# Performance work log

Measured on AMD Instinct MI355X. Metric: run time of the kernel, lower is better.

Reference implementation:

```python
import jax, jax.numpy as jnp
import numpy as np


def setup_inputs() -> dict:
    key = jax.random.key(0)
    k1, k2, k3 = jax.random.split(key, 3)
    B, C, H, W = 8, 256, 64, 64
    K = jax.random.normal(k1, (B, C, H, W), dtype=jnp.float32)
    Q = jax.random.normal(k2, (B, C, H, W), dtype=jnp.float32)
    V = jax.random.normal(k3, (B, C, H, W), dtype=jnp.float32)
    return {"K": K, "Q": Q, "V": V}


def reference(K, Q, V):
    # K, Q: [b, dim, h, w]; V: [b, v_dim, h, w]
    b, dim, h, w = K.shape
    v_dim = V.shape[1]
    hw = h * w
    Qf = jnp.transpose(K.reshape(b, dim, hw), (0, 2, 1)) * 0  # placeholder removed below
    Qf = jnp.transpose(Q.reshape(b, dim, hw), (0, 2, 1))  # [b, hw, dim]
    Kf = K.reshape(b, dim, hw)                              # [b, dim, hw]
    Vf = jnp.transpose(V.reshape(b, v_dim, hw), (0, 2, 1))  # [b, hw, v_dim]
    scores = jnp.einsum('bqd,bdk->bqk', Qf, Kf)             # [b, hw_q, hw_k]
    # NOTE: softmax over the QUERY axis (dim=1), matching the torch code
    att = jax.nn.softmax(scores, axis=1)
    out = jnp.einsum('bqk,bkv->bqv', att, Vf)               # [b, hw, v_dim]
    out = out.reshape(b, h, w, v_dim)
    return jnp.transpose(out, (0, 3, 1, 2))                 # [b, v_dim, h, w]
```

## Files before the change

kernel.cpp:

```cpp
#include <hip/hip_runtime.h>

#define HW   4096
#define DIM  256
#define NB   8

typedef short bf16x8 __attribute__((ext_vector_type(8)));
typedef short s16x4  __attribute__((ext_vector_type(4)));
typedef float f32x4  __attribute__((ext_vector_type(4)));
typedef float f32x16 __attribute__((ext_vector_type(16)));
typedef unsigned int u32;
typedef unsigned int u32_g __attribute__((address_space(1)));
typedef unsigned int u32_l __attribute__((address_space(3)));

__device__ __forceinline__ void split_bf16(float x, short& hi, short& lo) {
    unsigned u  = __builtin_bit_cast(unsigned, x);
    unsigned rh = (u + 0x7FFFu + ((u >> 16) & 1u)) >> 16;
    hi = (short)rh;
    float hf  = __builtin_bit_cast(float, rh << 16);
    float rem = x - hf;
    unsigned u2 = __builtin_bit_cast(unsigned, rem);
    unsigned rl = (u2 + 0x7FFFu + ((u2 >> 16) & 1u)) >> 16;
    lo = (short)rl;
}

__device__ __forceinline__ f32x4 mfma16(bf16x8 a, bf16x8 b, f32x4 c) {
    return __builtin_amdgcn_mfma_f32_16x16x32_bf16(a, b, c, 0, 0, 0);
}
__device__ __forceinline__ f32x16 mfma32(bf16x8 a, bf16x8 b, f32x16 c) {
    return __builtin_amdgcn_mfma_f32_32x32x16_bf16(a, b, c, 0, 0, 0);
}

__device__ __forceinline__ void gload16(const void* g, void* l) {
    __builtin_amdgcn_global_load_lds((const u32_g*)g, (u32_l*)l, 16, 0, 0);
}

extern "C" __global__ void __launch_bounds__(256)
pass0_T(const float* __restrict__ src, short* __restrict__ dsth,
        short* __restrict__ dstl)
{
    __shared__ __attribute__((aligned(16))) short TH[16][264];
    __shared__ __attribute__((aligned(16))) short TL[16][264];
    const int b   = blockIdx.y;
    const int hw0 = blockIdx.x * 16;
    const int t   = threadIdx.x;
    const float* sb = src + (size_t)b * DIM * HW;

    {
        const int rl = t & 15;
        const int dl = t >> 4;
        #pragma unroll
        for (int dp = 0; dp < 16; ++dp) {
            int d = dl + dp * 16;
            float x = sb[(size_t)d * HW + hw0 + rl];
            short h, l; split_bf16(x, h, l);
            TH[rl][d] = h; TL[rl][d] = l;
        }
    }
    __syncthreads();

    const int r   = t >> 4;
    const int c0  = (t & 15) * 2;
    const int swz = (r & 7) << 4;
    size_t rowbyte = ((size_t)b * HW + hw0 + r) * (size_t)(DIM * 2);
    char* dh = (char*)dsth + rowbyte;
    char* dl = (char*)dstl + rowbyte;
    #pragma unroll
    for (int j = 0; j < 2; ++j) {
        int cb  = (c0 + j) * 16;
        int cbs = cb ^ swz;
        *(f32x4*)(dh + cbs) = *(const f32x4*)((const char*)&TH[r][0] + cb);
        *(f32x4*)(dl + cbs) = *(const f32x4*)((const char*)&TL[r][0] + cb);
    }
}

extern "C" __global__ void __launch_bounds__(256)
pass0_V(const float* __restrict__ V, short* __restrict__ v2)
{
    const int b = blockIdx.y, v = blockIdx.x, t = threadIdx.x;
    const float* sv = V + ((size_t)b * DIM + v) * HW + t * 16;
    #pragma unroll
    for (int s = 0; s < 2; ++s) {
        f32x4 x0 = *(const f32x4*)(sv + s * 8);
        f32x4 x1 = *(const f32x4*)(sv + s * 8 + 4);
        s16x4 h0, l0, h1, l1;
        #pragma unroll
        for (int j = 0; j < 4; ++j) {
            short h, l;
            split_bf16(x0[j], h, l); h0[j] = h; l0[j] = l;
            split_bf16(x1[j], h, l); h1[j] = h; l1[j] = l;
        }
        short* dp = v2 + (((size_t)b * 512 + (size_t)(t * 2 + s)) * DIM + v) * 16;
        *(s16x4*)(dp + 0)  = h0;
        *(s16x4*)(dp + 4)  = h1;
        *(s16x4*)(dp + 8)  = l0;
        *(s16x4*)(dp + 12) = l1;
    }
}

extern "C" __global__ void __launch_bounds__(512, 2)
k3_stats(const short* __restrict__ KTh, const short* __restrict__ KTl,
         const short* __restrict__ QTh, const short* __restrict__ QTl,
         float* __restrict__ m_out, float* __restrict__ il_out)
{
    __shared__ __attribute__((aligned(16))) short QH[2][64][256];
    __shared__ __attribute__((aligned(16))) short QL[2][64][256];

    const int id   = blockIdx.x;
    const int b    = id & 7;
    const int k0b  = (id >> 3) * 128;
    const int t    = threadIdx.x;
    const int lane = t & 63;
    const int w    = t >> 6;
    const int g    = lane >> 4;
    const int lq   = lane & 15;

    bf16x8 kh[8], kl[8];
    {
        const int krow = k0b + w * 16 + lq;
        const char* rh = (const char*)KTh + ((size_t)b * HW + krow) * 512;
        const char* rl = (const char*)KTl + ((size_t)b * HW + krow) * 512;
        const int swz = (lq & 7) << 4;
        #pragma unroll
        for (int ds = 0; ds < 8; ++ds) {
            int cb = (64 * ds + 16 * g) ^ swz;
            kh[ds] = *(const bf16x8*)(rh + cb);
            kl[ds] = *(const bf16x8*)(rl + cb);
        }
    }

    const char* qhbase = (const char*)QTh + (size_t)b * HW * 512;
    const char* qlbase = (const char*)QTl + (size_t)b * HW * 512;
    auto stage = [&](int bi, int q0) {
        #pragma unroll
        for (int j = 0; j < 4; ++j) {
            int c = (j << 3) + w;
            int o = c * 1024;
            gload16(qhbase + (size_t)q0 * 512 + o + lane * 16,
                    (char*)&QH[bi][0][0] + o);
            gload16(qlbase + (size_t)q0 * 512 + o + lane * 16,
                    (char*)&QL[bi][0][0] + o);
        }
    };

    float mr[4], lr[4];
    #pragma unroll
    for (int r = 0; r < 4; ++r) { mr[r] = -3.0e38f; lr[r] = 0.0f; }

    stage(0, 0);
    __syncthreads();

    for (int it = 0; it < 64; ++it) {
        const int cur = it & 1;
        if (it + 1 < 64) stage(cur ^ 1, (it + 1) * 64);

        #pragma unroll
        for (int qt = 0; qt < 4; ++qt) {
            const int qr = qt * 16 + lq;
            const char* bhr = (const char*)&QH[cur][qr][0];
            const char* blr = (const char*)&QL[cur][qr][0];
            const int swzq = (qr & 7) << 4;
            f32x4 acc = {0.f, 0.f, 0.f, 0.f};
            __builtin_amdgcn_s_setprio(1);
            #pragma unroll
            for (int ds = 0; ds < 8; ++ds) {
                int cb = (64 * ds + 16 * g) ^ swzq;
                bf16x8 bh = *(const bf16x8*)(bhr + cb);
                bf16x8 bl = *(const bf16x8*)(blr + cb);
                acc = mfma16(kh[ds], bh, acc);
                acc = mfma16(kh[ds], bl, acc);
                acc = mfma16(kl[ds], bh, acc);
            }
            __builtin_amdgcn_s_setprio(0);
            #pragma unroll
            for (int r = 0; r < 4; ++r) {
                float s = acc[r];
                if (s > mr[r]) {
                    lr[r] = lr[r] * __expf(mr[r] - s) + 1.0f;
                    mr[r] = s;
                } else {
                    lr[r] += __expf(s - mr[r]);
                }
            }
        }
        __syncthreads();
    }

    #pragma unroll
    for (int r = 0; r < 4; ++r) {
        float m = mr[r], l = lr[r];
        #pragma unroll
        for (int off = 1; off < 16; off <<= 1) {
            float m2 = __shfl_xor(m, off);
            float l2 = __shfl_xor(l, off);
            float mn = fmaxf(m, m2);
            l = l * __expf(m - mn) + l2 * __expf(m2 - mn);
            m = mn;
        }
        if (lq == 0) {
            int kg = k0b + w * 16 + g * 4 + r;
            m_out[b * HW + kg]  = m;
            il_out[b * HW + kg] = 1.0f / l;
        }
    }
}

extern "C" __global__ void __launch_bounds__(512, 2)
k3_out(const short* __restrict__ KTh, const short* __restrict__ KTl,
       const short* __restrict__ QTh, const short* __restrict__ QTl,
       const short* __restrict__ V2,
       const float* __restrict__ m_in, const float* __restrict__ il_in,
       float* __restrict__ out)
{
    __shared__ __attribute__((aligned(16))) short KH[2][32][256];
    __shared__ __attribute__((aligned(16))) short KL[2][32][256];
    __shared__ __attribute__((aligned(16))) short PH[2][128][36];
    __shared__ __attribute__((aligned(16))) short PL[2][128][36];

    const int id   = blockIdx.x;
    const int b    = id & 7;
    const int q0   = (id >> 3) * 128;
    const int t    = threadIdx.x;
    const int lane = t & 63;
    const int w    = t >> 6;
    const int g    = lane >> 4;
    const int lq   = lane & 15;
    const int g2   = lane >> 5;
    const int l32  = lane & 31;
    const int wv   = w >> 1;
    const int wq2  = w & 1;

    bf16x8 qh[8], ql[8];
    {
        const int qrow = q0 + w * 16 + lq;
        const char* rh = (const char*)QTh + ((size_t)b * HW + qrow) * 512;
        const char* rl = (const char*)QTl + ((size_t)b * HW + qrow) * 512;
        const int swz = (lq & 7) << 4;
        #pragma unroll
        for (int ds = 0; ds < 8; ++ds) {
            int cb = (64 * ds + 16 * g) ^ swz;
            qh[ds] = *(const bf16x8*)(rh + cb);
            ql[ds] = *(const bf16x8*)(rl + cb);
        }
    }

    const char* khbase = (const char*)KTh + (size_t)b * HW * 512;
    const char* klbase = (const char*)KTl + (size_t)b * HW * 512;
    auto stage = [&](int bi, int k0a) {
        #pragma unroll
        for (int j = 0; j < 2; ++j) {
            int c = (j << 3) + w;
            int o = c * 1024;
            gload16(khbase + (size_t)k0a * 512 + o + lane * 16,
                    (char*)&KH[bi][0][0] + o);
            gload16(klbase + (size_t)k0a * 512 + o + lane * 16,
                    (char*)&KL[bi][0][0] + o);
        }
    };

    f32x16 acc[2][2];
    #pragma unroll
    for (int i = 0; i < 2; ++i)
        #pragma unroll
        for (int j = 0; j < 2; ++j)
            #pragma unroll
            for (int e = 0; e < 16; ++e) acc[i][j][e] = 0.0f;

    const float* mB  = m_in  + b * HW;
    const float* ilB = il_in + b * HW;

    stage(0, 0);
    __syncthreads();

    for (int it = 0; it < 128; ++it) {
        const int cur = it & 1;
        const int k0  = it * 32;

        if (it + 1 < 128) stage(cur ^ 1, k0 + 32);

        f32x4 mv[2], iv[2];
        #pragma unroll
        for (int kt = 0; kt < 2; ++kt) {
            mv[kt] = *(const f32x4*)&mB[k0 + kt * 16 + g * 4];
            iv[kt] = *(const f32x4*)&ilB[k0 + kt * 16 + g * 4];
        }

        bf16x8 vfh[2][2], vfl[2][2];
        #pragma unroll
        for (int kc = 0; kc < 2; ++kc) {
            const int seg = (k0 >> 3) + kc * 2 + g2;
            #pragma unroll
            for (int mt = 0; mt < 2; ++mt) {
                const int v = wv * 64 + mt * 32 + l32;
                const short* vp = V2 + (((size_t)b * 512 + seg) * DIM + v) * 16;
                vfh[kc][mt] = *(const bf16x8*)(vp);
                vfl[kc][mt] = *(const bf16x8*)(vp + 8);
            }
        }

        f32x4 sacc[2];
        #pragma unroll
        for (int kt = 0; kt < 2; ++kt) { f32x4 z = {0.f,0.f,0.f,0.f}; sacc[kt] = z; }
        const int swzk = (lq & 7) << 4;
        const char* ahr0 = (const char*)&KH[cur][lq][0];
        const char* ahr1 = (const char*)&KH[cur][16 + lq][0];
        const char* alr0 = (const char*)&KL[cur][lq][0];
        const char* alr1 = (const char*)&KL[cur][16 + lq][0];
        __builtin_amdgcn_s_setprio(1);
        #pragma unroll
        for (int ds = 0; ds < 8; ++ds) {
            int cb = (64 * ds + 16 * g) ^ swzk;
            {
                bf16x8 ah = *(const bf16x8*)(ahr0 + cb);
                bf16x8 al = *(const bf16x8*)(alr0 + cb);
                sacc[0] = mfma16(ah, qh[ds], sacc[0]);
                sacc[0] = mfma16(ah, ql[ds], sacc[0]);
                sacc[0] = mfma16(al, qh[ds], sacc[0]);
            }
            {
                bf16x8 ah = *(const bf16x8*)(ahr1 + cb);
                bf16x8 al = *(const bf16x8*)(alr1 + cb);
                sacc[1] = mfma16(ah, qh[ds], sacc[1]);
                sacc[1] = mfma16(ah, ql[ds], sacc[1]);
                sacc[1] = mfma16(al, qh[ds], sacc[1]);
            }
        }
        __builtin_amdgcn_s_setprio(0);

        {
            const int qc = w * 16 + lq;
            #pragma unroll
            for (int kt = 0; kt < 2; ++kt) {
                s16x4 ph, pl;
                #pragma unroll
                for (int r = 0; r < 4; ++r) {
                    float p = __expf(sacc[kt][r] - mv[kt][r]) * iv[kt][r];
                    short h, l; split_bf16(p, h, l);
                    ph[r] = h; pl[r] = l;
                }
                *(s16x4*)&PH[cur][qc][kt * 16 + g * 4] = ph;
                *(s16x4*)&PL[cur][qc][kt * 16 + g * 4] = pl;
            }
        }

        __syncthreads();

        __builtin_amdgcn_s_setprio(1);
        #pragma unroll
        for (int kc = 0; kc < 2; ++kc) {
            bf16x8 pbh[2], pbl[2];
            #pragma unroll
            for (int qt = 0; qt < 2; ++qt) {
                const int prow = wq2 * 64 + qt * 32 + l32;
                const short* p0 = &PH[cur][prow][kc * 16 + g2 * 8];
                const short* p1 = &PL[cur][prow][kc * 16 + g2 * 8];
                s16x4 a0 = *(const s16x4*)(p0);
                s16x4 a1 = *(const s16x4*)(p0 + 4);
                s16x4 b0 = *(const s16x4*)(p1);
                s16x4 b1 = *(const s16x4*)(p1 + 4);
                bf16x8 rh, rl;
                #pragma unroll
                for (int e = 0; e < 4; ++e) {
                    rh[e] = a0[e]; rh[4 + e] = a1[e];
                    rl[e] = b0[e]; rl[4 + e] = b1[e];
                }
                pbh[qt] = rh; pbl[qt] = rl;
            }
            #pragma unroll
            for (int mt = 0; mt < 2; ++mt) {
                #pragma unroll
                for (int qt = 0; qt < 2; ++qt) {
                    acc[mt][qt] = mfma32(vfh[kc][mt], pbh[qt], acc[mt][qt]);
                    acc[mt][qt] = mfma32(vfh[kc][mt], pbl[qt], acc[mt][qt]);
                    acc[mt][qt] = mfma32(vfl[kc][mt], pbh[qt], acc[mt][qt]);
                }
            }
        }
        __builtin_amdgcn_s_setprio(0);
    }

    float* __restrict__ ob = out + (size_t)b * DIM * HW;
    #pragma unroll
    for (int mt = 0; mt < 2; ++mt)
        #pragma unroll
        for (int qt = 0; qt < 2; ++qt)
            #pragma unroll
            for (int r = 0; r < 16; ++r) {
                int v = wv * 64 + mt * 32 + (r & 3) + 8 * (r >> 2) + 4 * g2;
                int q = q0 + wq2 * 64 + qt * 32 + l32;
                ob[(size_t)v * HW + q] = acc[mt][qt][r];
            }
}

extern "C" __global__ void __launch_bounds__(256, 1)
k_stats(const float* __restrict__ K, const float* __restrict__ Q,
        float* __restrict__ m_out, float* __restrict__ il_out)
{
    __shared__ __attribute__((aligned(16))) short KtH[64][264];
    __shared__ __attribute__((aligned(16))) short KtL[64][264];
    __shared__ __attribute__((aligned(16))) short QtH[32][264];
    __shared__ __attribute__((aligned(16))) short QtL[32][264];

    const int b = blockIdx.y, k0 = blockIdx.x * 64, t = threadIdx.x;
    const int lane = t & 63, w = t >> 6, g = lane >> 4, lq = lane & 15;
    const float* Kb = K + (size_t)b * DIM * HW;
    const float* Qb = Q + (size_t)b * DIM * HW;

    {
        const int kk = t & 63, d0 = t >> 6;
        #pragma unroll 4
        for (int pass = 0; pass < 64; ++pass) {
            int d = d0 + pass * 4;
            float x = Kb[(size_t)d * HW + k0 + kk];
            short h, l; split_bf16(x, h, l);
            KtH[kk][d] = h; KtL[kk][d] = l;
        }
    }
    float mr[4], lr[4];
    #pragma unroll
    for (int r = 0; r < 4; ++r) { mr[r] = -3.0e38f; lr[r] = 0.0f; }

    for (int q0 = 0; q0 < HW; q0 += 32) {
        __syncthreads();
        {
            const int qq = t & 31, d0 = t >> 5;
            #pragma unroll 4
            for (int pass = 0; pass < 32; ++pass) {
                int d = d0 + pass * 8;
                float x = Qb[(size_t)d * HW + q0 + qq];
                short h, l; split_bf16(x, h, l);
                QtH[qq][d] = h; QtL[qq][d] = l;
            }
        }
        __syncthreads();
        #pragma unroll
        for (int qt = 0; qt < 2; ++qt) {
            f32x4 acc = {0.f, 0.f, 0.f, 0.f};
            #pragma unroll
            for (int ds = 0; ds < 8; ++ds) {
                const int dof = ds * 32 + g * 8;
                bf16x8 ah = *(const bf16x8*)&KtH[w * 16 + lq][dof];
                bf16x8 al = *(const bf16x8*)&KtL[w * 16 + lq][dof];
                bf16x8 bh = *(const bf16x8*)&QtH[qt * 16 + lq][dof];
                bf16x8 bl = *(const bf16x8*)&QtL[qt * 16 + lq][dof];
                acc = mfma16(ah, bh, acc);
                acc = mfma16(ah, bl, acc);
                acc = mfma16(al, bh, acc);
            }
            #pragma unroll
            for (int r = 0; r < 4; ++r) {
                float s = acc[r];
                if (s > mr[r]) { lr[r] = lr[r] * __expf(mr[r] - s) + 1.0f; mr[r] = s; }
                else lr[r] += __expf(s - mr[r]);
            }
        }
    }
    #pragma unroll
    for (int r = 0; r < 4; ++r) {
        float m = mr[r], l = lr[r];
        #pragma unroll
        for (int off = 1; off < 16; off <<= 1) {
            float m2 = __shfl_xor(m, off), l2 = __shfl_xor(l, off);
            float mn = fmaxf(m, m2);
            l = l * __expf(m - mn) + l2 * __expf(m2 - mn);
            m = mn;
        }
        if (lq == 0) {
            int kg = k0 + w * 16 + g * 4 + r;
            m_out[b * HW + kg] = m;
            il_out[b * HW + kg] = 1.0f / l;
        }
    }
}

extern "C" __global__ void __launch_bounds__(256, 1)
k_attn_out(const float* __restrict__ K, const float* __restrict__ Q,
           const float* __restrict__ V,
           const float* __restrict__ m_in, const float* __restrict__ il_in,
           float* __restrict__ out)
{
    __shared__ __attribute__((aligned(16))) short QtH[64][264];
    __shared__ __attribute__((aligned(16))) short QtL[64][264];
    __shared__ __attribute__((aligned(16))) short KtH[32][264];
    __shared__ __attribute__((aligned(16))) short KtL[32][264];
    __shared__ __attribute__((aligned(16))) short PtH[64][40];
    __shared__ __attribute__((aligned(16))) short PtL[64][40];

    const int b = blockIdx.y, q0 = blockIdx.x * 64, t = threadIdx.x;
    const int lane = t & 63, w = t >> 6, g = lane >> 4, lq = lane & 15;
    const int g2 = lane >> 5, l32 = lane & 31;
    const float* Kb = K + (size_t)b * DIM * HW;
    const float* Qb = Q + (size_t)b * DIM * HW;
    const float* Vb = V + (size_t)b * DIM * HW;
    const float* mB = m_in + b * HW;
    const float* ilB = il_in + b * HW;

    {
        const int qq = t & 63, d0 = t >> 6;
        #pragma unroll 4
        for (int pass = 0; pass < 64; ++pass) {
            int d = d0 + pass * 4;
            float x = Qb[(size_t)d * HW + q0 + qq];
            short h, l; split_bf16(x, h, l);
            QtH[qq][d] = h; QtL[qq][d] = l;
        }
    }
    f32x16 acc[2][2];
    #pragma unroll
    for (int i = 0; i < 2; ++i)
        #pragma unroll
        for (int j = 0; j < 2; ++j)
            #pragma unroll
            for (int e = 0; e < 16; ++e) acc[i][j][e] = 0.0f;

    for (int k0 = 0; k0 < HW; k0 += 32) {
        __syncthreads();
        {
            const int kk = t & 31, d0 = t >> 5;
            #pragma unroll 4
            for (int pass = 0; pass < 32; ++pass) {
                int d = d0 + pass * 8;
                float x = Kb[(size_t)d * HW + k0 + kk];
                short h, l; split_bf16(x, h, l);
                KtH[kk][d] = h; KtL[kk][d] = l;
            }
        }
        __syncthreads();
        f32x4 sacc[2];
        #pragma unroll
        for (int kt = 0; kt < 2; ++kt) { f32x4 z = {0.f,0.f,0.f,0.f}; sacc[kt] = z; }
        #pragma unroll
        for (int ds = 0; ds < 8; ++ds) {
            const int dof = ds * 32 + g * 8;
            bf16x8 bh = *(const bf16x8*)&QtH[w * 16 + lq][dof];
            bf16x8 bl = *(const bf16x8*)&QtL[w * 16 + lq][dof];
            #pragma unroll
            for (int kt = 0; kt < 2; ++kt) {
                bf16x8 ah = *(const bf16x8*)&KtH[kt * 16 + lq][dof];
                bf16x8 al = *(const bf16x8*)&KtL[kt * 16 + lq][dof];
                sacc[kt] = mfma16(ah, bh, sacc[kt]);
                sacc[kt] = mfma16(ah, bl, sacc[kt]);
                sacc[kt] = mfma16(al, bh, sacc[kt]);
            }
        }
        {
            const int qc = w * 16 + lq;
            #pragma unroll
            for (int kt = 0; kt < 2; ++kt) {
                s16x4 ph, pl;
                #pragma unroll
                for (int r = 0; r < 4; ++r) {
                    int kg = k0 + kt * 16 + g * 4 + r;
                    float p = __expf(sacc[kt][r] - mB[kg]) * ilB[kg];
                    short h, l; split_bf16(p, h, l);
                    ph[r] = h; pl[r] = l;
                }
                *(s16x4*)&PtH[qc][kt * 16 + g * 4] = ph;
                *(s16x4*)&PtL[qc][kt * 16 + g * 4] = pl;
            }
        }
        __syncthreads();
        #pragma unroll
        for (int kc = 0; kc < 2; ++kc) {
            bf16x8 pbh[2], pbl[2];
            #pragma unroll
            for (int qt = 0; qt < 2; ++qt) {
                pbh[qt] = *(const bf16x8*)&PtH[qt * 32 + l32][kc * 16 + g2 * 8];
                pbl[qt] = *(const bf16x8*)&PtL[qt * 32 + l32][kc * 16 + g2 * 8];
            }
            #pragma unroll
            for (int mt = 0; mt < 2; ++mt) {
                const int v = w * 64 + mt * 32 + l32;
                const float* vp = Vb + (size_t)v * HW + k0 + kc * 16 + g2 * 8;
                f32x4 x0 = *(const f32x4*)vp;
                f32x4 x1 = *(const f32x4*)(vp + 4);
                bf16x8 ah, al;
                #pragma unroll
                for (int j = 0; j < 4; ++j) {
                    short h, l;
                    split_bf16(x0[j], h, l); ah[j] = h;     al[j] = l;
                    split_bf16(x1[j], h, l); ah[4 + j] = h; al[4 + j] = l;
                }
                #pragma unroll
                for (int qt = 0; qt < 2; ++qt) {
                    acc[mt][qt] = mfma32(ah, pbh[qt], acc[mt][qt]);
                    acc[mt][qt] = mfma32(ah, pbl[qt], acc[mt][qt]);
                    acc[mt][qt] = mfma32(al, pbh[qt], acc[mt][qt]);
                }
            }
        }
    }
    float* ob = out + (size_t)b * DIM * HW;
    #pragma unroll
    for (int mt = 0; mt < 2; ++mt)
        #pragma unroll
        for (int qt = 0; qt < 2; ++qt)
            #pragma unroll
            for (int r = 0; r < 16; ++r) {
                int v = w * 64 + mt * 32 + (r & 3) + 8 * (r >> 2) + 4 * g2;
                int q = q0 + qt * 32 + l32;
                ob[(size_t)v * HW + q] = acc[mt][qt][r];
            }
}

extern "C" void kernel_launch(void* const* d_in, const int* in_sizes, int n_in,
                              void* d_out, int out_size, void* d_ws, size_t ws_size,
                              hipStream_t stream)
{
    (void)in_sizes; (void)n_in; (void)out_size;
    const float* K = (const float*)d_in[0];
    const float* Q = (const float*)d_in[1];
    const float* V = (const float*)d_in[2];

    char* wsb = (char*)d_ws;
    float* m_ws  = (float*)wsb;
    float* il_ws = m_ws + (size_t)NB * HW;

    const size_t planeElems = (size_t)NB * HW * DIM;
    const size_t statsBytes = 262144;
    const size_t need = statsBytes + planeElems * 2 * 4
                                   + planeElems * 2 * 2 ;

    dim3 blk(256);
    if (ws_size >= need) {
        short* KTh = (short*)(wsb + statsBytes);
        short* KTl = KTh + planeElems;
        short* QTh = KTl + planeElems;
        short* QTl = QTh + planeElems;
        short* V2  = QTl + planeElems;

        dim3 gT(HW / 16, NB);
        pass0_T<<<gT, blk, 0, stream>>>(K, KTh, KTl);
        pass0_T<<<gT, blk, 0, stream>>>(Q, QTh, QTl);
        dim3 gV(DIM, NB);
        pass0_V<<<gV, blk, 0, stream>>>(V, V2);

        dim3 blk5(512);
        k3_stats<<<dim3(256), blk5, 0, stream>>>(KTh, KTl, QTh, QTl, m_ws, il_ws);
        k3_out<<<dim3(256), blk5, 0, stream>>>(KTh, KTl, QTh, QTl, V2,
                                               m_ws, il_ws, (float*)d_out);
    } else {
        dim3 gM(64, NB);
        k_stats<<<gM, blk, 0, stream>>>(K, Q, m_ws, il_ws);
        k_attn_out<<<gM, blk, 0, stream>>>(K, Q, V, m_ws, il_ws, (float*)d_out);
    }
}
```

Measured before the change: 638.3 us.

## Switch attention stats and output kernels to 32x32 MFMA tiles with larger K chunks

Both the stats and output kernels move their score GEMM from 16x16x32 to 32x32x16 MFMA tiles. Each wave now covers 32 keys by 32 queries and holds 16 register fragments per operand. The stats kernel adds an LDS merge of partial max/sum across two query-half waves. The output kernel processes 64 keys per iteration with a single-buffered K tile, loads m/il through async LDS loads, and reads P fragments with wider vector loads. The aim is fewer loop iterations, fewer LDS fragment reads per MFMA and better MFMA efficiency. The cost is higher register pressure and an extra barrier per iteration, since the K loads now follow the score compute instead of being double-buffered.

```diff
diff --git a/kernel.cpp b/kernel.cpp
--- a/kernel.cpp
+++ b/kernel.cpp
@@ -8,7 +8,6 @@
 typedef short s16x4  __attribute__((ext_vector_type(4)));
 typedef float f32x4  __attribute__((ext_vector_type(4)));
 typedef float f32x16 __attribute__((ext_vector_type(16)));
-typedef unsigned int u32;
 typedef unsigned int u32_g __attribute__((address_space(1)));
 typedef unsigned int u32_l __attribute__((address_space(3)));
 
@@ -32,6 +31,9 @@
 
 __device__ __forceinline__ void gload16(const void* g, void* l) {
     __builtin_amdgcn_global_load_lds((const u32_g*)g, (u32_l*)l, 16, 0, 0);
+}
+__device__ __forceinline__ void gload4(const void* g, void* l) {
+    __builtin_amdgcn_global_load_lds((const u32_g*)g, (u32_l*)l, 4, 0, 0);
 }
 
 extern "C" __global__ void __launch_bounds__(256)
@@ -98,12 +100,13 @@
 }
 
 extern "C" __global__ void __launch_bounds__(512, 2)
-k3_stats(const short* __restrict__ KTh, const short* __restrict__ KTl,
+k4_stats(const short* __restrict__ KTh, const short* __restrict__ KTl,
          const short* __restrict__ QTh, const short* __restrict__ QTl,
          float* __restrict__ m_out, float* __restrict__ il_out)
 {
     __shared__ __attribute__((aligned(16))) short QH[2][64][256];
     __shared__ __attribute__((aligned(16))) short QL[2][64][256];
+    __shared__ __attribute__((aligned(16))) float MRG[2][128][2];
 
     const int id   = blockIdx.x;
     const int b    = id & 7;
@@ -111,20 +114,22 @@
     const int t    = threadIdx.x;
     const int lane = t & 63;
     const int w    = t >> 6;
-    const int g    = lane >> 4;
-    const int lq   = lane & 15;
-
-    bf16x8 kh[8], kl[8];
+    const int l32  = lane & 31;
+    const int g2   = lane >> 5;
+    const int wk   = w >> 1;
+    const int wq   = w & 1;
+
+    bf16x8 kh[16], kl[16];
     {
-        const int krow = k0b + w * 16 + lq;
+        const int krow = k0b + wk * 32 + l32;
         const char* rh = (const char*)KTh + ((size_t)b * HW + krow) * 512;
         const char* rl = (const char*)KTl + ((size_t)b * HW + krow) * 512;
-        const int swz = (lq & 7) << 4;
-        #pragma unroll
-        for (int ds = 0; ds < 8; ++ds) {
-            int cb = (64 * ds + 16 * g) ^ swz;
-            kh[ds] = *(const bf16x8*)(rh + cb);
-            kl[ds] = *(const bf16x8*)(rl + cb);
+        const int swz = (l32 & 7) << 4;
+        #pragma unroll
+        for (int s = 0; s < 16; ++s) {
+            int cb = (s * 32 + g2 * 16) ^ swz;
+            kh[s] = *(const bf16x8*)(rh + cb);
+            kl[s] = *(const bf16x8*)(rl + cb);
         }
     }
 
@@ -133,8 +138,8 @@
     auto stage = [&](int bi, int q0) {
         #pragma unroll
         for (int j = 0; j < 4; ++j) {
-            int c = (j << 3) + w;
-            int o = c * 1024;
+            int cc = (j << 3) + w;
+            int o  = cc * 1024;
             gload16(qhbase + (size_t)q0 * 512 + o + lane * 16,
                     (char*)&QH[bi][0][0] + o);
             gload16(qlbase + (size_t)q0 * 512 + o + lane * 16,
@@ -142,79 +147,92 @@
         }
     };
 
-    float mr[4], lr[4];
-    #pragma unroll
-    for (int r = 0; r < 4; ++r) { mr[r] = -3.0e38f; lr[r] = 0.0f; }
+    float mr[16], lr[16];
+    #pragma unroll
+    for (int r = 0; r < 16; ++r) { mr[r] = -3.0e38f; lr[r] = 0.0f; }
 
     stage(0, 0);
     __syncthreads();
+
+    const int qrow = wq * 32 + l32;
+    const int qswz = (qrow & 7) << 4;
 
     for (int it = 0; it < 64; ++it) {
         const int cur = it & 1;
         if (it + 1 < 64) stage(cur ^ 1, (it + 1) * 64);
 
-        #pragma unroll
-        for (int qt = 0; qt < 4; ++qt) {
-            const int qr = qt * 16 + lq;
-            const char* bhr = (const char*)&QH[cur][qr][0];
-            const char* blr = (const char*)&QL[cur][qr][0];
-            const int swzq = (qr & 7) << 4;
-            f32x4 acc = {0.f, 0.f, 0.f, 0.f};
-            __builtin_amdgcn_s_setprio(1);
-            #pragma unroll
-            for (int ds = 0; ds < 8; ++ds) {
-                int cb = (64 * ds + 16 * g) ^ swzq;
-                bf16x8 bh = *(const bf16x8*)(bhr + cb);
-                bf16x8 bl = *(const bf16x8*)(blr + cb);
-                acc = mfma16(kh[ds], bh, acc);
-                acc = mfma16(kh[ds], bl, acc);
-                acc = mfma16(kl[ds], bh, acc);
-            }
-            __builtin_amdgcn_s_setprio(0);
-            #pragma unroll
-            for (int r = 0; r < 4; ++r) {
-                float s = acc[r];
-                if (s > mr[r]) {
-                    lr[r] = lr[r] * __expf(mr[r] - s) + 1.0f;
-                    mr[r] = s;
-                } else {
-                    lr[r] += __expf(s - mr[r]);
-                }
-            }
-        }
-        __syncthreads();
-    }
-
-    #pragma unroll
-    for (int r = 0; r < 4; ++r) {
+        const char* bhr = (const char*)&QH[cur][qrow][0];
+        const char* blr = (const char*)&QL[cur][qrow][0];
+        f32x16 c1, c2;
+        #pragma unroll
+        for (int e = 0; e < 16; ++e) { c1[e] = 0.0f; c2[e] = 0.0f; }
+
+        __builtin_amdgcn_s_setprio(1);
+        #pragma unroll
+        for (int s = 0; s < 16; ++s) {
+            int cb = (s * 32 + g2 * 16) ^ qswz;
+            bf16x8 bh = *(const bf16x8*)(bhr + cb);
+            bf16x8 bl = *(const bf16x8*)(blr + cb);
+            c1 = mfma32(kh[s], bh, c1);
+            c1 = mfma32(kh[s], bl, c1);
+            c2 = mfma32(kl[s], bh, c2);
+        }
+        __builtin_amdgcn_s_setprio(0);
+
+        #pragma unroll
+        for (int r = 0; r < 16; ++r) {
+            float sv = c1[r] + c2[r];
+            float nm = fmaxf(mr[r], sv);
+            lr[r] = lr[r] * __expf(mr[r] - nm) + __expf(sv - nm);
+            mr[r] = nm;
+        }
+        __syncthreads();
+    }
+
+    #pragma unroll
+    for (int r = 0; r < 16; ++r) {
         float m = mr[r], l = lr[r];
         #pragma unroll
-        for (int off = 1; off < 16; off <<= 1) {
+        for (int off = 1; off < 32; off <<= 1) {
             float m2 = __shfl_xor(m, off);
             float l2 = __shfl_xor(l, off);
-            float mn = fmaxf(m, m2);
-            l = l * __expf(m - mn) + l2 * __expf(m2 - mn);
-            m = mn;
-        }
-        if (lq == 0) {
-            int kg = k0b + w * 16 + g * 4 + r;
-            m_out[b * HW + kg]  = m;
-            il_out[b * HW + kg] = 1.0f / l;
-        }
+            float nm = fmaxf(m, m2);
+            l = l * __expf(m - nm) + l2 * __expf(m2 - nm);
+            m = nm;
+        }
+        mr[r] = m; lr[r] = l;
+    }
+    if (l32 == 0) {
+        #pragma unroll
+        for (int r = 0; r < 16; ++r) {
+            int klo = wk * 32 + 4 * g2 + (r & 3) + 8 * (r >> 2);
+            MRG[wq][klo][0] = mr[r];
+            MRG[wq][klo][1] = lr[r];
+        }
+    }
+    __syncthreads();
+    if (t < 128) {
+        float m0 = MRG[0][t][0], l0 = MRG[0][t][1];
+        float m1 = MRG[1][t][0], l1 = MRG[1][t][1];
+        float nm = fmaxf(m0, m1);
+        float l  = l0 * __expf(m0 - nm) + l1 * __expf(m1 - nm);
+        m_out[b * HW + k0b + t]  = nm;
+        il_out[b * HW + k0b + t] = 1.0f / l;
     }
 }
 
 extern "C" __global__ void __launch_bounds__(512, 2)
-k3_out(const short* __restrict__ KTh, const short* __restrict__ KTl,
+k4_out(const short* __restrict__ KTh, const short* __restrict__ KTl,
        const short* __restrict__ QTh, const short* __restrict__ QTl,
        const short* __restrict__ V2,
        const float* __restrict__ m_in, const float* __restrict__ il_in,
        float* __restrict__ out)
 {
-    __shared__ __attribute__((aligned(16))) short KH[2][32][256];
-    __shared__ __attribute__((aligned(16))) short KL[2][32][256];
-    __shared__ __attribute__((aligned(16))) short PH[2][128][36];
-    __shared__ __attribute__((aligned(16))) short PL[2][128][36];
+    __shared__ __attribute__((aligned(16))) short KH[64][256];
+    __shared__ __attribute__((aligned(16))) short KL[64][256];
+    __shared__ __attribute__((aligned(16))) short PH[128][72];
+    __shared__ __attribute__((aligned(16))) short PL[128][72];
+    __shared__ __attribute__((aligned(16))) float MI[2][128];
 
     const int id   = blockIdx.x;
     const int b    = id & 7;
@@ -222,156 +240,136 @@
     const int t    = threadIdx.x;
     const int lane = t & 63;
     const int w    = t >> 6;
-    const int g    = lane >> 4;
-    const int lq   = lane & 15;
+    const int l32  = lane & 31;
     const int g2   = lane >> 5;
-    const int l32  = lane & 31;
+    const int a    = w & 1;
+    const int c    = w >> 1;
     const int wv   = w >> 1;
     const int wq2  = w & 1;
 
-    bf16x8 qh[8], ql[8];
+    bf16x8 qh[16], ql[16];
     {
-        const int qrow = q0 + w * 16 + lq;
+        const int qrow = q0 + c * 32 + l32;
         const char* rh = (const char*)QTh + ((size_t)b * HW + qrow) * 512;
         const char* rl = (const char*)QTl + ((size_t)b * HW + qrow) * 512;
-        const int swz = (lq & 7) << 4;
-        #pragma unroll
-        for (int ds = 0; ds < 8; ++ds) {
-            int cb = (64 * ds + 16 * g) ^ swz;
-            qh[ds] = *(const bf16x8*)(rh + cb);
-            ql[ds] = *(const bf16x8*)(rl + cb);
+        const int swz = (l32 & 7) << 4;
+        #pragma unroll
+        for (int s = 0; s < 16; ++s) {
+            int cb = (s * 32 + g2 * 16) ^ swz;
+            qh[s] = *(const bf16x8*)(rh + cb);
+            ql[s] = *(const bf16x8*)(rl + cb);
         }
     }
 
     const char* khbase = (const char*)KTh + (size_t)b * HW * 512;
     const char* klbase = (const char*)KTl + (size_t)b * HW * 512;
-    auto stage = [&](int bi, int k0a) {
-        #pragma unroll
-        for (int j = 0; j < 2; ++j) {
-            int c = (j << 3) + w;
-            int o = c * 1024;
-            gload16(khbase + (size_t)k0a * 512 + o + lane * 16,
-                    (char*)&KH[bi][0][0] + o);
-            gload16(klbase + (size_t)k0a * 512 + o + lane * 16,
-                    (char*)&KL[bi][0][0] + o);
+    auto stageK = [&](int k0s) {
+        #pragma unroll
+        for (int j = 0; j < 4; ++j) {
+            int cc = (j << 3) + w;
+            int o  = cc * 1024;
+            gload16(khbase + (size_t)k0s * 512 + o + lane * 16,
+                    (char*)&KH[0][0] + o);
+            gload16(klbase + (size_t)k0s * 512 + o + lane * 16,
+                    (char*)&KL[0][0] + o);
         }
     };
-
-    f32x16 acc[2][2];
-    #pragma unroll
-    for (int i = 0; i < 2; ++i)
-        #pragma unroll
-        for (int j = 0; j < 2; ++j)
-            #pragma unroll
-            for (int e = 0; e < 16; ++e) acc[i][j][e] = 0.0f;
-
     const float* mB  = m_in  + b * HW;
     const float* ilB = il_in + b * HW;
-
-    stage(0, 0);
+    auto stageMI = [&](int bi, int k0s) {
+        if (w == 0) {
+            gload4(mB  + k0s + lane, (char*)&MI[bi][0]);
+            gload4(ilB + k0s + lane, (char*)&MI[bi][64]);
+        }
+    };
+
+    f32x16 acc[2][2];
+    #pragma unroll
+    for (int i = 0; i < 2; ++i)
+        #pragma unroll
+        for (int j = 0; j < 2; ++j)
+            #pragma unroll
+            for (int e = 0; e < 16; ++e) acc[i][j][e] = 0.0f;
+
+    stageK(0);
+    stageMI(0, 0);
     __syncthreads();
 
-    for (int it = 0; it < 128; ++it) {
+    const int arow = a * 32 + l32;
+    const int aswz = (l32 & 7) << 4;
+    const char* ahr = (const char*)&KH[arow][0];
+    const char* alr = (const char*)&KL[arow][0];
+    const int prow = c * 32 + l32;
+
+    for (int it = 0; it < 64; ++it) {
         const int cur = it & 1;
-        const int k0  = it * 32;
-
-        if (it + 1 < 128) stage(cur ^ 1, k0 + 32);
-
-        f32x4 mv[2], iv[2];
-        #pragma unroll
-        for (int kt = 0; kt < 2; ++kt) {
-            mv[kt] = *(const f32x4*)&mB[k0 + kt * 16 + g * 4];
-            iv[kt] = *(const f32x4*)&ilB[k0 + kt * 16 + g * 4];
-        }
-
-        bf16x8 vfh[2][2], vfl[2][2];
-        #pragma unroll
-        for (int kc = 0; kc < 2; ++kc) {
-            const int seg = (k0 >> 3) + kc * 2 + g2;
+        const int k0  = it * 64;
+
+        f32x16 c1, c2;
+        #pragma unroll
+        for (int e = 0; e < 16; ++e) { c1[e] = 0.0f; c2[e] = 0.0f; }
+
+        __builtin_amdgcn_s_setprio(1);
+        #pragma unroll
+        for (int s = 0; s < 16; ++s) {
+            int cb = (s * 32 + g2 * 16) ^ aswz;
+            bf16x8 ah = *(const bf16x8*)(ahr + cb);
+            bf16x8 al = *(const bf16x8*)(alr + cb);
+            c1 = mfma32(ah, qh[s], c1);
+            c1 = mfma32(ah, ql[s], c1);
+            c2 = mfma32(al, qh[s], c2);
+        }
+        __builtin_amdgcn_s_setprio(0);
+
+        __syncthreads();
+
+        if (it + 1 < 64) {
+            stageK(k0 + 64);
+            stageMI(cur ^ 1, k0 + 64);
+        }
+
+        #pragma unroll
+        for (int run = 0; run < 4; ++run) {
+            int idx = a * 32 + 4 * g2 + 8 * run;
+            f32x4 m4 = *(const f32x4*)&MI[cur][idx];
+            f32x4 i4 = *(const f32x4*)&MI[cur][64 + idx];
+            s16x4 ph, pl;
+            #pragma unroll
+            for (int e = 0; e < 4; ++e) {
+                int r = run * 4 + e;
+                float sv = c1[r] + c2[r];
+                float p  = __expf(sv - m4[e]) * i4[e];
+                short h, l; split_bf16(p, h, l);
+                ph[e] = h; pl[e] = l;
+            }
+            *(s16x4*)&PH[prow][idx] = ph;
+            *(s16x4*)&PL[prow][idx] = pl;
+        }
+
+        __syncthreads();
+
+        __builtin_amdgcn_s_setprio(1);
+        #pragma unroll
+        for (int kc = 0; kc < 4; ++kc) {
+            bf16x8 pbh[2], pbl[2];
+            #pragma unroll
+            for (int qt = 0; qt < 2; ++qt) {
+                int pr = wq2 * 64 + qt * 32 + l32;
+                pbh[qt] = *(const bf16x8*)&PH[pr][kc * 16 + g2 * 8];
+                pbl[qt] = *(const bf16x8*)&PL[pr][kc * 16 + g2 * 8];
+            }
+            const int seg = it * 8 + kc * 2 + g2;
             #pragma unroll
             for (int mt = 0; mt < 2; ++mt) {
-                const int v = wv * 64 + mt * 32 + l32;
+                int v = wv * 64 + mt * 32 + l32;
                 const short* vp = V2 + (((size_t)b * 512 + seg) * DIM + v) * 16;
-                vfh[kc][mt] = *(const bf16x8*)(vp);
-                vfl[kc][mt] = *(const bf16x8*)(vp + 8);
-            }
-        }
-
-        f32x4 sacc[2];
-        #pragma unroll
-        for (int kt = 0; kt < 2; ++kt) { f32x4 z = {0.f,0.f,0.f,0.f}; sacc[kt] = z; }
-        const int swzk = (lq & 7) << 4;
-        const char* ahr0 = (const char*)&KH[cur][lq][0];
-        const char* ahr1 = (const char*)&KH[cur][16 + lq][0];
-        const char* alr0 = (const char*)&KL[cur][lq][0];
-        const char* alr1 = (const char*)&KL[cur][16 + lq][0];
-        __builtin_amdgcn_s_setprio(1);
-        #pragma unroll
-        for (int ds = 0; ds < 8; ++ds) {
-            int cb = (64 * ds + 16 * g) ^ swzk;
-            {
-                bf16x8 ah = *(const bf16x8*)(ahr0 + cb);
-                bf16x8 al = *(const bf16x8*)(alr0 + cb);
-                sacc[0] = mfma16(ah, qh[ds], sacc[0]);
-                sacc[0] = mfma16(ah, ql[ds], sacc[0]);
-                sacc[0] = mfma16(al, qh[ds], sacc[0]);
-            }
-            {
-                bf16x8 ah = *(const bf16x8*)(ahr1 + cb);
-                bf16x8 al = *(const bf16x8*)(alr1 + cb);
-                sacc[1] = mfma16(ah, qh[ds], sacc[1]);
-                sacc[1] = mfma16(ah, ql[ds], sacc[1]);
-                sacc[1] = mfma16(al, qh[ds], sacc[1]);
-            }
-        }
-        __builtin_amdgcn_s_setprio(0);
-
-        {
-            const int qc = w * 16 + lq;
-            #pragma unroll
-            for (int kt = 0; kt < 2; ++kt) {
-                s16x4 ph, pl;
-                #pragma unroll
-                for (int r = 0; r < 4; ++r) {
-                    float p = __expf(sacc[kt][r] - mv[kt][r]) * iv[kt][r];
-                    short h, l; split_bf16(p, h, l);
-                    ph[r] = h; pl[r] = l;
-                }
-                *(s16x4*)&PH[cur][qc][kt * 16 + g * 4] = ph;
-                *(s16x4*)&PL[cur][qc][kt * 16 + g * 4] = pl;
-            }
-        }
-
-        __syncthreads();
-
-        __builtin_amdgcn_s_setprio(1);
-        #pragma unroll
-        for (int kc = 0; kc < 2; ++kc) {
-            bf16x8 pbh[2], pbl[2];
-            #pragma unroll
-            for (int qt = 0; qt < 2; ++qt) {
-                const int prow = wq2 * 64 + qt * 32 + l32;
-                const short* p0 = &PH[cur][prow][kc * 16 + g2 * 8];
-                const short* p1 = &PL[cur][prow][kc * 16 + g2 * 8];
-                s16x4 a0 = *(const s16x4*)(p0);
-                s16x4 a1 = *(const s16x4*)(p0 + 4);
-                s16x4 b0 = *(const s16x4*)(p1);
-                s16x4 b1 = *(const s16x4*)(p1 + 4);
-                bf16x8 rh, rl;
-                #pragma unroll
-                for (int e = 0; e < 4; ++e) {
-                    rh[e] = a0[e]; rh[4 + e] = a1[e];
-                    rl[e] = b0[e]; rl[4 + e] = b1[e];
-                }
-                pbh[qt] = rh; pbl[qt] = rl;
-            }
-            #pragma unroll
-            for (int mt = 0; mt < 2; ++mt) {
+                bf16x8 vh = *(const bf16x8*)(vp);
+                bf16x8 vl = *(const bf16x8*)(vp + 8);
                 #pragma unroll
                 for (int qt = 0; qt < 2; ++qt) {
-                    acc[mt][qt] = mfma32(vfh[kc][mt], pbh[qt], acc[mt][qt]);
-                    acc[mt][qt] = mfma32(vfh[kc][mt], pbl[qt], acc[mt][qt]);
-                    acc[mt][qt] = mfma32(vfl[kc][mt], pbh[qt], acc[mt][qt]);
+                    acc[mt][qt] = mfma32(vh, pbh[qt], acc[mt][qt]);
+                    acc[mt][qt] = mfma32(vh, pbl[qt], acc[mt][qt]);
+                    acc[mt][qt] = mfma32(vl, pbh[qt], acc[mt][qt]);
                 }
             }
         }
@@ -635,8 +633,8 @@
         pass0_V<<<gV, blk, 0, stream>>>(V, V2);
 
         dim3 blk5(512);
-        k3_stats<<<dim3(256), blk5, 0, stream>>>(KTh, KTl, QTh, QTl, m_ws, il_ws);
-        k3_out<<<dim3(256), blk5, 0, stream>>>(KTh, KTl, QTh, QTl, V2,
+        k4_stats<<<dim3(256), blk5, 0, stream>>>(KTh, KTl, QTh, QTl, m_ws, il_ws);
+        k4_out<<<dim3(256), blk5, 0, stream>>>(KTh, KTl, QTh, QTl, V2,
                                                m_ws, il_ws, (float*)d_out);
     } else {
         dim3 gM(64, NB);
```

Result: slower. 710.3 us (+11.3%).
